# Optimization experiments

Measured on AMD Instinct MI355X. Metric: run time of the kernel, lower is better.

Reference implementation:

```python
import jax, jax.numpy as jnp
import numpy as np

D_MODEL = 1024
H = 16
D_K = D_MODEL // H
B, S = 2, 2048

def setup_inputs() -> dict:
    key = jax.random.key(0)
    ks = jax.random.split(key, 13)
    scale = 1.0 / np.sqrt(D_MODEL)
    mk = lambda k: jax.random.normal(k, (D_MODEL, D_MODEL), dtype=jnp.float32) * scale
    return {
        'q': jax.random.normal(ks[0], (B, S, D_MODEL), dtype=jnp.float32),
        'k': jax.random.normal(ks[1], (B, S, D_MODEL), dtype=jnp.float32),
        'v': jax.random.normal(ks[2], (B, S, D_MODEL), dtype=jnp.float32),
        'mask': jax.random.randint(ks[3], (B, 1, S, S), 0, 2, dtype=jnp.int32),
        'wq': mk(ks[4]), 'bq': jnp.zeros((D_MODEL,), jnp.float32),
        'wk': mk(ks[5]), 'bk': jnp.zeros((D_MODEL,), jnp.float32),
        'wv': mk(ks[6]), 'bv': jnp.zeros((D_MODEL,), jnp.float32),
        'wo': mk(ks[7]), 'bo': jnp.zeros((D_MODEL,), jnp.float32),
    }

def reference(q, k, v, mask, wq, bq, wk, bk, wv, bv, wo, bo):
    b, s, _ = q.shape
    # linear projections then split heads: [B,S,D] -> [B,H,S,Dk]
    def proj(x, w, bias):
        y = x @ w + bias
        return y.reshape(b, -1, H, D_K).transpose(0, 2, 1, 3)
    Q = proj(q, wq, bq)
    K = proj(k, wk, bk)
    V = proj(v, wv, bv)
    scores = jnp.einsum('bhqd,bhkd->bhqk', Q, K) / jnp.sqrt(jnp.float32(D_K))
    # faithful to source: masked positions are set to 1e-9 (not -inf)
    scores = jnp.where(mask == 0, jnp.float32(1e-9), scores)
    attn = jax.nn.softmax(scores, axis=-1)  # dropout is identity in eval mode
    x = jnp.einsum('bhqk,bhkd->bhqd', attn, V)
    x = x.transpose(0, 2, 1, 3).reshape(b, s, D_MODEL)
    return x @ wo + bo
```

## Files before the change

### kernel.cpp

```cpp
#include <hip/hip_runtime.h>
#include <hip/hip_bf16.h>

#define DM 1024
#define HEADS 16
#define DKK 64
#define BB 2
#define SS 2048
#define MROWS (BB*SS)

typedef __attribute__((ext_vector_type(8))) short bf16x8;
typedef __attribute__((ext_vector_type(4))) float f32x4;
typedef __hip_bfloat16 bf16;

#define SC2 0.1803368801f
#define MB2 1.442695041e-9f

__device__ __forceinline__ void async16(const void* g, void* l) {
    __builtin_amdgcn_global_load_lds((const __attribute__((address_space(1))) void*)g,
                                     (__attribute__((address_space(3))) void*)l, 16, 0, 0);
}

__global__ void prep_kernel(const float* __restrict__ q, const float* __restrict__ k,
                            const float* __restrict__ v,
                            const float* __restrict__ wq, const float* __restrict__ wk,
                            const float* __restrict__ wv, const float* __restrict__ wo,
                            const int* __restrict__ mask,
                            bf16* __restrict__ qkv, bf16* __restrict__ wcat,
                            unsigned long long* __restrict__ bits) {
    __shared__ float tile[32][33];
    const int bid = blockIdx.x;
    const int tid = threadIdx.x;
    if (bid < 12288) {
        const int z = bid >> 12;
        const int i = ((bid & 4095) << 8) + tid;
        const float* src = z == 0 ? q : (z == 1 ? k : v);
        float4 val = ((const float4*)src)[i];
        union { bf16 b[4]; ushort4 u; } cvt;
        cvt.b[0] = __float2bfloat16(val.x);
        cvt.b[1] = __float2bfloat16(val.y);
        cvt.b[2] = __float2bfloat16(val.z);
        cvt.b[3] = __float2bfloat16(val.w);
        ((ushort4*)(qkv + (size_t)z * MROWS * DM))[i] = cvt.u;
    } else if (bid < 12288 + 4096) {
        const int t = bid - 12288;
        const int z = t >> 10;
        const int bx = t & 31, by = (t >> 5) & 31;
        const float* src = z == 0 ? wq : (z == 1 ? wk : (z == 2 ? wv : wo));
        bf16* dst = wcat + ((size_t)z << 20);
        const int tx = tid & 31, ty = tid >> 5;
        const int x = bx * 32 + tx, y0 = by * 32 + ty;
#pragma unroll
        for (int i = 0; i < 32; i += 8)
            tile[ty + i][tx] = src[(size_t)(y0 + i) * DM + x];
        __syncthreads();
        const int nx = by * 32 + tx, ny0 = bx * 32 + ty;
#pragma unroll
        for (int i = 0; i < 32; i += 8)
            dst[(size_t)(ny0 + i) * DM + nx] = __float2bfloat16(tile[tx][ty + i]);
    } else {
        const int i = ((bid - 16384) << 8) + tid;
        unsigned long long b = __ballot(mask[i] != 0);
        if ((tid & 63) == 0) bits[i >> 6] = b;
    }
}

__global__ __launch_bounds__(256) void gemm_qkv(const bf16* __restrict__ qb, const bf16* __restrict__ kb,
                                                const bf16* __restrict__ vb, const bf16* __restrict__ wcat,
                                                const float* __restrict__ bq, const float* __restrict__ bk,
                                                const float* __restrict__ bv,
                                                bf16* __restrict__ Qh, bf16* __restrict__ Kh,
                                                bf16* __restrict__ Vt) {
    __shared__ __align__(16) bf16 lA[128 * 32];
    __shared__ __align__(16) bf16 lB[128 * 32];
    const int seg = blockIdx.x >> 3;
    const bf16* A    = seg == 0 ? qb : (seg == 1 ? kb : vb);
    const bf16* Bt   = wcat + ((size_t)seg << 20);
    const float* bias = seg == 0 ? bq : (seg == 1 ? bk : bv);

    const int tid  = threadIdx.x;
    const int lane = tid & 63;
    const int lm   = lane & 15;
    const int quad = lane >> 4;
    const int w    = tid >> 6;
    const int wm   = w >> 1, wn = w & 1;
    const int m0   = blockIdx.y * 128;
    const int n0   = (blockIdx.x & 7) * 128;
    const int wbase = w << 6;

    f32x4 acc[4][4];
#pragma unroll
    for (int i = 0; i < 4; ++i)
#pragma unroll
        for (int j = 0; j < 4; ++j) acc[i][j] = (f32x4){0.f, 0.f, 0.f, 0.f};

    for (int kt = 0; kt < DM / 32; ++kt) {
#pragma unroll
        for (int r = 0; r < 2; ++r) {
            const int idx = r * 256 + tid;
            const int row = idx >> 2;
            const int kc  = idx & 3;
            async16(A + (size_t)(m0 + row) * DM + kt * 32 + kc * 8,
                    (char*)lA + (size_t)(r * 256 + wbase) * 16);
            async16(Bt + (size_t)(n0 + row) * DM + kt * 32 + kc * 8,
                    (char*)lB + (size_t)(r * 256 + wbase) * 16);
        }
        __syncthreads();
        bf16x8 af[4], bb[4];
#pragma unroll
        for (int mt = 0; mt < 4; ++mt)
            af[mt] = *(const bf16x8*)&lA[(wm * 64 + mt * 16 + lm) * 32 + quad * 8];
#pragma unroll
        for (int nt = 0; nt < 4; ++nt)
            bb[nt] = *(const bf16x8*)&lB[(wn * 64 + nt * 16 + lm) * 32 + quad * 8];
#pragma unroll
        for (int mt = 0; mt < 4; ++mt)
#pragma unroll
            for (int nt = 0; nt < 4; ++nt)
                acc[mt][nt] = __builtin_amdgcn_mfma_f32_16x16x32_bf16(af[mt], bb[nt], acc[mt][nt], 0, 0, 0);
        __syncthreads();
    }

    bf16* outQK = seg == 0 ? Qh : Kh;
    const float oscale = (seg == 1) ? SC2 : 1.0f;
#pragma unroll
    for (int mt = 0; mt < 4; ++mt) {
#pragma unroll
        for (int nt = 0; nt < 4; ++nt) {
            const int gcol = n0 + wn * 64 + nt * 16 + lm;
            const float bvv = bias[gcol];
            const int h = gcol >> 6, d = gcol & 63;
#pragma unroll
            for (int r = 0; r < 4; ++r) {
                const int grow = m0 + wm * 64 + mt * 16 + quad * 4 + r;
                const int b = grow >> 11, s = grow & 2047;
                const float val = (acc[mt][nt][r] + bvv) * oscale;
                if (seg < 2)
                    outQK[((size_t)(b * HEADS + h) * SS + s) * DKK + d] = __float2bfloat16(val);
                else
                    Vt[((size_t)(b * HEADS + h) * DKK + d) * SS + s] = __float2bfloat16(val);
            }
        }
    }
}

__global__ __launch_bounds__(256) void gemm_out(const bf16* __restrict__ A, const bf16* __restrict__ Bt,
                                                const float* __restrict__ bias, float* __restrict__ outp) {
    __shared__ __align__(16) bf16 lA[128 * 32];
    __shared__ __align__(16) bf16 lB[64 * 32];
    const int tid  = threadIdx.x;
    const int lane = tid & 63;
    const int lm   = lane & 15;
    const int quad = lane >> 4;
    const int w    = tid >> 6;
    const int m0   = blockIdx.y * 128;
    const int n0   = blockIdx.x * 64;
    const int wbase = w << 6;

    f32x4 acc[2][4];
#pragma unroll
    for (int i = 0; i < 2; ++i)
#pragma unroll
        for (int j = 0; j < 4; ++j) acc[i][j] = (f32x4){0.f, 0.f, 0.f, 0.f};

    for (int kt = 0; kt < DM / 32; ++kt) {
#pragma unroll
        for (int r = 0; r < 2; ++r) {
            const int idx = r * 256 + tid;
            const int row = idx >> 2;
            const int kc  = idx & 3;
            async16(A + (size_t)(m0 + row) * DM + kt * 32 + kc * 8,
                    (char*)lA + (size_t)(r * 256 + wbase) * 16);
        }
        {
            const int row = tid >> 2;
            const int kc  = tid & 3;
            async16(Bt + (size_t)(n0 + row) * DM + kt * 32 + kc * 8,
                    (char*)lB + (size_t)(wbase) * 16);
        }
        __syncthreads();
        bf16x8 af[2], bb[4];
#pragma unroll
        for (int mt = 0; mt < 2; ++mt)
            af[mt] = *(const bf16x8*)&lA[(w * 32 + mt * 16 + lm) * 32 + quad * 8];
#pragma unroll
        for (int nt = 0; nt < 4; ++nt)
            bb[nt] = *(const bf16x8*)&lB[(nt * 16 + lm) * 32 + quad * 8];
#pragma unroll
        for (int mt = 0; mt < 2; ++mt)
#pragma unroll
            for (int nt = 0; nt < 4; ++nt)
                acc[mt][nt] = __builtin_amdgcn_mfma_f32_16x16x32_bf16(af[mt], bb[nt], acc[mt][nt], 0, 0, 0);
        __syncthreads();
    }

#pragma unroll
    for (int mt = 0; mt < 2; ++mt)
#pragma unroll
        for (int nt = 0; nt < 4; ++nt) {
            const int gcol = n0 + nt * 16 + lm;
            const float bvv = bias[gcol];
#pragma unroll
            for (int r = 0; r < 4; ++r) {
                const int grow = m0 + w * 32 + mt * 16 + quad * 4 + r;
                outp[(size_t)grow * DM + gcol] = acc[mt][nt][r] + bvv;
            }
        }
}

__global__ __launch_bounds__(256, 4) void attn_kernel(const bf16* __restrict__ Qh, const bf16* __restrict__ Kh,
                                                      const bf16* __restrict__ Vt,
                                                      const unsigned long long* __restrict__ mbits,
                                                      bf16* __restrict__ ctx) {
    __shared__ __align__(16) bf16 ldsK[2][64 * 64];
    __shared__ __align__(16) bf16 ldsV[2][64 * 64];
    __shared__ __align__(16) bf16 ldsP[4][16 * 64];

    const int tid  = threadIdx.x;
    const int lane = tid & 63;
    const int lm   = lane & 15;
    const int quad = lane >> 4;
    const int w    = tid >> 6;
    const int bh   = blockIdx.y;
    const int b    = bh >> 4;
    const int h    = bh & 15;
    const int q0   = blockIdx.x * 64;
    const int qrow = q0 + w * 16 + lm;

    const int x0 = quad ^ (lm & 7);
    const int x1 = x0 ^ 4;

    const int L0 = tid, L1 = 256 + tid;
    const int row0 = L0 >> 3, sw0 = (L0 & 7) ^ (row0 & 7);
    const int row1 = L1 >> 3, sw1 = (L1 & 7) ^ (row1 & 7);
    const bf16* kbase = Kh + (size_t)bh * SS * DKK;
    const bf16* vbase = Vt + (size_t)bh * DKK * SS;
    const bf16* pK0 = kbase + (size_t)row0 * DKK + sw0 * 8;
    const bf16* pK1 = kbase + (size_t)row1 * DKK + sw1 * 8;
    const bf16* pV0 = vbase + (size_t)row0 * SS + sw0 * 8;
    const bf16* pV1 = vbase + (size_t)row1 * SS + sw1 * 8;
    char* dKa[2] = { (char*)ldsK[0] + (size_t)(w * 64) * 16, (char*)ldsK[1] + (size_t)(w * 64) * 16 };
    char* dKb[2] = { (char*)ldsK[0] + (size_t)(256 + w * 64) * 16, (char*)ldsK[1] + (size_t)(256 + w * 64) * 16 };
    char* dVa[2] = { (char*)ldsV[0] + (size_t)(w * 64) * 16, (char*)ldsV[1] + (size_t)(w * 64) * 16 };
    char* dVb[2] = { (char*)ldsV[0] + (size_t)(256 + w * 64) * 16, (char*)ldsV[1] + (size_t)(256 + w * 64) * 16 };

    const bf16* qp = Qh + ((size_t)bh * SS + qrow) * DKK;
    const bf16x8 aq0 = *(const bf16x8*)(qp + quad * 8);
    const bf16x8 aq1 = *(const bf16x8*)(qp + 32 + quad * 8);

    const unsigned long long* pm = mbits + ((size_t)b * SS + qrow) * (SS / 64);

    f32x4 o[4];
#pragma unroll
    for (int i = 0; i < 4; ++i) o[i] = (f32x4){0.f, 0.f, 0.f, 0.f};
    float lsum = 0.f;
    bf16* pmy = &ldsP[w][0];

    async16(pK0, dKa[0]);
    async16(pK1, dKb[0]);
    async16(pV0, dVa[0]);
    async16(pV1, dVb[0]);
    __syncthreads();

    const int nkt = SS / 64;

    auto body = [&](int it, int cur) {
        const unsigned long long mw = pm[it];
        if (it + 1 < nkt) {
            const int nb = cur ^ 1;
            const size_t ko = (size_t)(it + 1) * 64;
            async16(pK0 + ko * DKK, dKa[nb]);
            async16(pK1 + ko * DKK, dKb[nb]);
            async16(pV0 + ko, dVa[nb]);
            async16(pV1 + ko, dVb[nb]);
        }
        const bf16* lk = ldsK[cur];
        const bf16* lv = ldsV[cur];

        f32x4 sc[4];
#pragma unroll
        for (int mt = 0; mt < 4; ++mt) {
            sc[mt] = (f32x4){0.f, 0.f, 0.f, 0.f};
            const bf16x8 kf0 = *(const bf16x8*)&lk[(mt * 16 + lm) * 64 + x0 * 8];
            const bf16x8 kf1 = *(const bf16x8*)&lk[(mt * 16 + lm) * 64 + x1 * 8];
            sc[mt] = __builtin_amdgcn_mfma_f32_16x16x32_bf16(kf0, aq0, sc[mt], 0, 0, 0);
            sc[mt] = __builtin_amdgcn_mfma_f32_16x16x32_bf16(kf1, aq1, sc[mt], 0, 0, 0);
        }

        const unsigned long long mq = mw >> (quad * 4);
#pragma unroll
        for (int mt = 0; mt < 4; ++mt) {
            const unsigned int mmt = (unsigned int)(mq >> (mt * 16));
            union { bf16 hh[4]; uint2 u; } pk;
#pragma unroll
            for (int r = 0; r < 4; ++r) {
                const float sv = ((mmt >> r) & 1u) ? sc[mt][r] : MB2;
                const float p = __builtin_amdgcn_exp2f(sv);
                lsum += p;
                pk.hh[r] = __float2bfloat16(p);
            }
            *(uint2*)&pmy[lm * 64 + (((mt * 2 + (quad >> 1)) ^ (lm & 7)) << 3) + ((quad & 1) << 2)] = pk.u;
        }

        const bf16x8 pf0 = *(const bf16x8*)&pmy[lm * 64 + x0 * 8];
        const bf16x8 pf1 = *(const bf16x8*)&pmy[lm * 64 + x1 * 8];
#pragma unroll
        for (int mt = 0; mt < 4; ++mt) {
            const bf16x8 vf0 = *(const bf16x8*)&lv[(mt * 16 + lm) * 64 + x0 * 8];
            const bf16x8 vf1 = *(const bf16x8*)&lv[(mt * 16 + lm) * 64 + x1 * 8];
            o[mt] = __builtin_amdgcn_mfma_f32_16x16x32_bf16(vf0, pf0, o[mt], 0, 0, 0);
            o[mt] = __builtin_amdgcn_mfma_f32_16x16x32_bf16(vf1, pf1, o[mt], 0, 0, 0);
        }

        __syncthreads();
    };

    for (int it = 0; it < nkt; it += 2) {
        body(it, 0);
        body(it + 1, 1);
    }

    lsum += __shfl_xor(lsum, 16);
    lsum += __shfl_xor(lsum, 32);
    const float rl = 1.0f / lsum;

    bf16* crow = ctx + ((size_t)b * SS + qrow) * DM + h * DKK;
#pragma unroll
    for (int mt = 0; mt < 4; ++mt) {
        union { bf16 hh[4]; uint2 u; } pk;
#pragma unroll
        for (int r = 0; r < 4; ++r) pk.hh[r] = __float2bfloat16(o[mt][r] * rl);
        *(uint2*)&crow[mt * 16 + quad * 4] = pk.u;
    }
}

extern "C" void kernel_launch(void* const* d_in, const int* in_sizes, int n_in,
                              void* d_out, int out_size, void* d_ws, size_t ws_size,
                              hipStream_t stream) {
    const float* q  = (const float*)d_in[0];
    const float* k  = (const float*)d_in[1];
    const float* v  = (const float*)d_in[2];
    const int* mask = (const int*)d_in[3];
    const float* wq = (const float*)d_in[4];
    const float* bq = (const float*)d_in[5];
    const float* wk = (const float*)d_in[6];
    const float* bk = (const float*)d_in[7];
    const float* wv = (const float*)d_in[8];
    const float* bv = (const float*)d_in[9];
    const float* wo = (const float*)d_in[10];
    const float* bo = (const float*)d_in[11];

    const size_t MB = 1ull << 20;
    char* ws = (char*)d_ws;
    bf16* qkv  = (bf16*)(ws + 0 * MB);
    bf16* wcat = (bf16*)(ws + 24 * MB);
    bf16* wot  = (bf16*)(ws + 30 * MB);
    bf16* Qh   = (bf16*)(ws + 32 * MB);
    bf16* Kh   = (bf16*)(ws + 40 * MB);
    bf16* Vt   = (bf16*)(ws + 48 * MB);
    bf16* ctx  = (bf16*)(ws + 56 * MB);
    unsigned long long* mbits = (unsigned long long*)(ws + 64 * MB);

    prep_kernel<<<49152, 256, 0, stream>>>(q, k, v, wq, wk, wv, wo, mask, qkv, wcat, mbits);

    gemm_qkv<<<dim3(24, 32), 256, 0, stream>>>(qkv, qkv + (size_t)MROWS * DM, qkv + 2 * (size_t)MROWS * DM,
                                               wcat, bq, bk, bv, Qh, Kh, Vt);

    attn_kernel<<<dim3(SS / 64, BB * HEADS), 256, 0, stream>>>(Qh, Kh, Vt, mbits, ctx);

    gemm_out<<<dim3(DM / 64, MROWS / 128), 256, 0, stream>>>(ctx, wot, bo, (float*)d_out);
}
```

Measured before the change: 273.4 us.

## Double-buffer GEMM LDS tiles and compute softmax row sums with MFMA

Both projection GEMMs now prefetch the next K tile into a second LDS buffer while computing on the current one, removing the per-iteration sync between issuing and consuming loads. In attention, the softmax denominator is accumulated via an extra MFMA with a ones operand instead of per-lane scalar adds and cross-lane shuffles. This costs double the LDS per GEMM block and two extra MFMAs per key tile.

```diff
diff --git a/kernel.cpp b/kernel.cpp
--- a/kernel.cpp
+++ b/kernel.cpp
@@ -70,8 +70,8 @@
                                                 const float* __restrict__ bv,
                                                 bf16* __restrict__ Qh, bf16* __restrict__ Kh,
                                                 bf16* __restrict__ Vt) {
-    __shared__ __align__(16) bf16 lA[128 * 32];
-    __shared__ __align__(16) bf16 lB[128 * 32];
+    __shared__ __align__(16) bf16 lA[2][128 * 32];
+    __shared__ __align__(16) bf16 lB[2][128 * 32];
     const int seg = blockIdx.x >> 3;
     const bf16* A    = seg == 0 ? qb : (seg == 1 ? kb : vb);
     const bf16* Bt   = wcat + ((size_t)seg << 20);
@@ -93,25 +93,33 @@
 #pragma unroll
         for (int j = 0; j < 4; ++j) acc[i][j] = (f32x4){0.f, 0.f, 0.f, 0.f};
 
-    for (int kt = 0; kt < DM / 32; ++kt) {
+    auto stage = [&](int kt, int buf) {
 #pragma unroll
         for (int r = 0; r < 2; ++r) {
             const int idx = r * 256 + tid;
             const int row = idx >> 2;
             const int kc  = idx & 3;
             async16(A + (size_t)(m0 + row) * DM + kt * 32 + kc * 8,
-                    (char*)lA + (size_t)(r * 256 + wbase) * 16);
+                    (char*)lA[buf] + (size_t)(r * 256 + wbase) * 16);
             async16(Bt + (size_t)(n0 + row) * DM + kt * 32 + kc * 8,
-                    (char*)lB + (size_t)(r * 256 + wbase) * 16);
-        }
-        __syncthreads();
+                    (char*)lB[buf] + (size_t)(r * 256 + wbase) * 16);
+        }
+    };
+
+    stage(0, 0);
+    __syncthreads();
+
+    const int nkt = DM / 32;
+    for (int kt = 0; kt < nkt; ++kt) {
+        const int cur = kt & 1;
+        if (kt + 1 < nkt) stage(kt + 1, cur ^ 1);
         bf16x8 af[4], bb[4];
 #pragma unroll
         for (int mt = 0; mt < 4; ++mt)
-            af[mt] = *(const bf16x8*)&lA[(wm * 64 + mt * 16 + lm) * 32 + quad * 8];
+            af[mt] = *(const bf16x8*)&lA[cur][(wm * 64 + mt * 16 + lm) * 32 + quad * 8];
 #pragma unroll
         for (int nt = 0; nt < 4; ++nt)
-            bb[nt] = *(const bf16x8*)&lB[(wn * 64 + nt * 16 + lm) * 32 + quad * 8];
+            bb[nt] = *(const bf16x8*)&lB[cur][(wn * 64 + nt * 16 + lm) * 32 + quad * 8];
 #pragma unroll
         for (int mt = 0; mt < 4; ++mt)
 #pragma unroll
@@ -145,8 +153,8 @@
 
 __global__ __launch_bounds__(256) void gemm_out(const bf16* __restrict__ A, const bf16* __restrict__ Bt,
                                                 const float* __restrict__ bias, float* __restrict__ outp) {
-    __shared__ __align__(16) bf16 lA[128 * 32];
-    __shared__ __align__(16) bf16 lB[64 * 32];
+    __shared__ __align__(16) bf16 lA[2][128 * 32];
+    __shared__ __align__(16) bf16 lB[2][64 * 32];
     const int tid  = threadIdx.x;
     const int lane = tid & 63;
     const int lm   = lane & 15;
@@ -162,29 +170,37 @@
 #pragma unroll
         for (int j = 0; j < 4; ++j) acc[i][j] = (f32x4){0.f, 0.f, 0.f, 0.f};
 
-    for (int kt = 0; kt < DM / 32; ++kt) {
+    auto stage = [&](int kt, int buf) {
 #pragma unroll
         for (int r = 0; r < 2; ++r) {
             const int idx = r * 256 + tid;
             const int row = idx >> 2;
             const int kc  = idx & 3;
             async16(A + (size_t)(m0 + row) * DM + kt * 32 + kc * 8,
-                    (char*)lA + (size_t)(r * 256 + wbase) * 16);
+                    (char*)lA[buf] + (size_t)(r * 256 + wbase) * 16);
         }
         {
             const int row = tid >> 2;
             const int kc  = tid & 3;
             async16(Bt + (size_t)(n0 + row) * DM + kt * 32 + kc * 8,
-                    (char*)lB + (size_t)(wbase) * 16);
-        }
-        __syncthreads();
+                    (char*)lB[buf] + (size_t)wbase * 16);
+        }
+    };
+
+    stage(0, 0);
+    __syncthreads();
+
+    const int nkt = DM / 32;
+    for (int kt = 0; kt < nkt; ++kt) {
+        const int cur = kt & 1;
+        if (kt + 1 < nkt) stage(kt + 1, cur ^ 1);
         bf16x8 af[2], bb[4];
 #pragma unroll
         for (int mt = 0; mt < 2; ++mt)
-            af[mt] = *(const bf16x8*)&lA[(w * 32 + mt * 16 + lm) * 32 + quad * 8];
+            af[mt] = *(const bf16x8*)&lA[cur][(w * 32 + mt * 16 + lm) * 32 + quad * 8];
 #pragma unroll
         for (int nt = 0; nt < 4; ++nt)
-            bb[nt] = *(const bf16x8*)&lB[(nt * 16 + lm) * 32 + quad * 8];
+            bb[nt] = *(const bf16x8*)&lB[cur][(nt * 16 + lm) * 32 + quad * 8];
 #pragma unroll
         for (int mt = 0; mt < 2; ++mt)
 #pragma unroll
@@ -249,10 +265,14 @@
 
     const unsigned long long* pm = mbits + ((size_t)b * SS + qrow) * (SS / 64);
 
+    const short one_bf16 = (short)0x3F80;
+    const bf16x8 onesf = (bf16x8){one_bf16, one_bf16, one_bf16, one_bf16,
+                                  one_bf16, one_bf16, one_bf16, one_bf16};
+
     f32x4 o[4];
 #pragma unroll
     for (int i = 0; i < 4; ++i) o[i] = (f32x4){0.f, 0.f, 0.f, 0.f};
-    float lsum = 0.f;
+    f32x4 o5 = (f32x4){0.f, 0.f, 0.f, 0.f};
     bf16* pmy = &ldsP[w][0];
 
     async16(pK0, dKa[0]);
@@ -294,9 +314,7 @@
 #pragma unroll
             for (int r = 0; r < 4; ++r) {
                 const float sv = ((mmt >> r) & 1u) ? sc[mt][r] : MB2;
-                const float p = __builtin_amdgcn_exp2f(sv);
-                lsum += p;
-                pk.hh[r] = __float2bfloat16(p);
+                pk.hh[r] = __float2bfloat16(__builtin_amdgcn_exp2f(sv));
             }
             *(uint2*)&pmy[lm * 64 + (((mt * 2 + (quad >> 1)) ^ (lm & 7)) << 3) + ((quad & 1) << 2)] = pk.u;
         }
@@ -310,6 +328,8 @@
             o[mt] = __builtin_amdgcn_mfma_f32_16x16x32_bf16(vf0, pf0, o[mt], 0, 0, 0);
             o[mt] = __builtin_amdgcn_mfma_f32_16x16x32_bf16(vf1, pf1, o[mt], 0, 0, 0);
         }
+        o5 = __builtin_amdgcn_mfma_f32_16x16x32_bf16(onesf, pf0, o5, 0, 0, 0);
+        o5 = __builtin_amdgcn_mfma_f32_16x16x32_bf16(onesf, pf1, o5, 0, 0, 0);
 
         __syncthreads();
     };
@@ -319,9 +339,7 @@
         body(it + 1, 1);
     }
 
-    lsum += __shfl_xor(lsum, 16);
-    lsum += __shfl_xor(lsum, 32);
-    const float rl = 1.0f / lsum;
+    const float rl = 1.0f / o5[0];
 
     bf16* crow = ctx + ((size_t)b * SS + qrow) * DM + h * DKK;
 #pragma unroll
```

After: 280.8 us. +2.7%, slower.

## Double attention query tile to 128 rows and compute row sums via MFMA

Applied to the files above, without the earlier changes.

The attention kernel now runs 512 threads (8 waves) per block, each block covering 128 query rows. Each K/V tile loaded into LDS is therefore shared by twice as many queries, and each thread issues one async load per tile instead of two. The softmax denominator is no longer accumulated with scalar adds and a cross-lane shuffle reduction. It comes from an extra MFMA against a ones vector using the bf16 probabilities, which adds two MFMAs per tile and sums bf16-rounded values instead of fp32 ones. The grid shrinks to half as many blocks, and the larger blocks may reduce occupancy.

```diff
diff --git a/kernel.cpp b/kernel.cpp
--- a/kernel.cpp
+++ b/kernel.cpp
@@ -175,7 +175,7 @@
             const int row = tid >> 2;
             const int kc  = tid & 3;
             async16(Bt + (size_t)(n0 + row) * DM + kt * 32 + kc * 8,
-                    (char*)lB + (size_t)(wbase) * 16);
+                    (char*)lB + (size_t)wbase * 16);
         }
         __syncthreads();
         bf16x8 af[2], bb[4];
@@ -207,13 +207,13 @@
         }
 }
 
-__global__ __launch_bounds__(256, 4) void attn_kernel(const bf16* __restrict__ Qh, const bf16* __restrict__ Kh,
+__global__ __launch_bounds__(512, 4) void attn_kernel(const bf16* __restrict__ Qh, const bf16* __restrict__ Kh,
                                                       const bf16* __restrict__ Vt,
                                                       const unsigned long long* __restrict__ mbits,
                                                       bf16* __restrict__ ctx) {
     __shared__ __align__(16) bf16 ldsK[2][64 * 64];
     __shared__ __align__(16) bf16 ldsV[2][64 * 64];
-    __shared__ __align__(16) bf16 ldsP[4][16 * 64];
+    __shared__ __align__(16) bf16 ldsP[8][16 * 64];
 
     const int tid  = threadIdx.x;
     const int lane = tid & 63;
@@ -223,25 +223,19 @@
     const int bh   = blockIdx.y;
     const int b    = bh >> 4;
     const int h    = bh & 15;
-    const int q0   = blockIdx.x * 64;
+    const int q0   = blockIdx.x * 128;
     const int qrow = q0 + w * 16 + lm;
 
     const int x0 = quad ^ (lm & 7);
     const int x1 = x0 ^ 4;
 
-    const int L0 = tid, L1 = 256 + tid;
-    const int row0 = L0 >> 3, sw0 = (L0 & 7) ^ (row0 & 7);
-    const int row1 = L1 >> 3, sw1 = (L1 & 7) ^ (row1 & 7);
+    const int row = tid >> 3, sw = (tid & 7) ^ (row & 7);
     const bf16* kbase = Kh + (size_t)bh * SS * DKK;
     const bf16* vbase = Vt + (size_t)bh * DKK * SS;
-    const bf16* pK0 = kbase + (size_t)row0 * DKK + sw0 * 8;
-    const bf16* pK1 = kbase + (size_t)row1 * DKK + sw1 * 8;
-    const bf16* pV0 = vbase + (size_t)row0 * SS + sw0 * 8;
-    const bf16* pV1 = vbase + (size_t)row1 * SS + sw1 * 8;
-    char* dKa[2] = { (char*)ldsK[0] + (size_t)(w * 64) * 16, (char*)ldsK[1] + (size_t)(w * 64) * 16 };
-    char* dKb[2] = { (char*)ldsK[0] + (size_t)(256 + w * 64) * 16, (char*)ldsK[1] + (size_t)(256 + w * 64) * 16 };
-    char* dVa[2] = { (char*)ldsV[0] + (size_t)(w * 64) * 16, (char*)ldsV[1] + (size_t)(w * 64) * 16 };
-    char* dVb[2] = { (char*)ldsV[0] + (size_t)(256 + w * 64) * 16, (char*)ldsV[1] + (size_t)(256 + w * 64) * 16 };
+    const bf16* pK = kbase + (size_t)row * DKK + sw * 8;
+    const bf16* pV = vbase + (size_t)row * SS + sw * 8;
+    char* dK[2] = { (char*)ldsK[0] + (size_t)w * 1024, (char*)ldsK[1] + (size_t)w * 1024 };
+    char* dV[2] = { (char*)ldsV[0] + (size_t)w * 1024, (char*)ldsV[1] + (size_t)w * 1024 };
 
     const bf16* qp = Qh + ((size_t)bh * SS + qrow) * DKK;
     const bf16x8 aq0 = *(const bf16x8*)(qp + quad * 8);
@@ -249,16 +243,18 @@
 
     const unsigned long long* pm = mbits + ((size_t)b * SS + qrow) * (SS / 64);
 
+    const short one_bf16 = (short)0x3F80;
+    const bf16x8 onesf = (bf16x8){one_bf16, one_bf16, one_bf16, one_bf16,
+                                  one_bf16, one_bf16, one_bf16, one_bf16};
+
     f32x4 o[4];
 #pragma unroll
     for (int i = 0; i < 4; ++i) o[i] = (f32x4){0.f, 0.f, 0.f, 0.f};
-    float lsum = 0.f;
+    f32x4 o5 = (f32x4){0.f, 0.f, 0.f, 0.f};
     bf16* pmy = &ldsP[w][0];
 
-    async16(pK0, dKa[0]);
-    async16(pK1, dKb[0]);
-    async16(pV0, dVa[0]);
-    async16(pV1, dVb[0]);
+    async16(pK, dK[0]);
+    async16(pV, dV[0]);
     __syncthreads();
 
     const int nkt = SS / 64;
@@ -268,10 +264,8 @@
         if (it + 1 < nkt) {
             const int nb = cur ^ 1;
             const size_t ko = (size_t)(it + 1) * 64;
-            async16(pK0 + ko * DKK, dKa[nb]);
-            async16(pK1 + ko * DKK, dKb[nb]);
-            async16(pV0 + ko, dVa[nb]);
-            async16(pV1 + ko, dVb[nb]);
+            async16(pK + ko * DKK, dK[nb]);
+            async16(pV + ko, dV[nb]);
         }
         const bf16* lk = ldsK[cur];
         const bf16* lv = ldsV[cur];
@@ -294,9 +288,7 @@
 #pragma unroll
             for (int r = 0; r < 4; ++r) {
                 const float sv = ((mmt >> r) & 1u) ? sc[mt][r] : MB2;
-                const float p = __builtin_amdgcn_exp2f(sv);
-                lsum += p;
-                pk.hh[r] = __float2bfloat16(p);
+                pk.hh[r] = __float2bfloat16(__builtin_amdgcn_exp2f(sv));
             }
             *(uint2*)&pmy[lm * 64 + (((mt * 2 + (quad >> 1)) ^ (lm & 7)) << 3) + ((quad & 1) << 2)] = pk.u;
         }
@@ -310,6 +302,8 @@
             o[mt] = __builtin_amdgcn_mfma_f32_16x16x32_bf16(vf0, pf0, o[mt], 0, 0, 0);
             o[mt] = __builtin_amdgcn_mfma_f32_16x16x32_bf16(vf1, pf1, o[mt], 0, 0, 0);
         }
+        o5 = __builtin_amdgcn_mfma_f32_16x16x32_bf16(onesf, pf0, o5, 0, 0, 0);
+        o5 = __builtin_amdgcn_mfma_f32_16x16x32_bf16(onesf, pf1, o5, 0, 0, 0);
 
         __syncthreads();
     };
@@ -319,9 +313,7 @@
         body(it + 1, 1);
     }
 
-    lsum += __shfl_xor(lsum, 16);
-    lsum += __shfl_xor(lsum, 32);
-    const float rl = 1.0f / lsum;
+    const float rl = 1.0f / o5[0];
 
     bf16* crow = ctx + ((size_t)b * SS + qrow) * DM + h * DKK;
 #pragma unroll
@@ -365,7 +357,7 @@
     gemm_qkv<<<dim3(24, 32), 256, 0, stream>>>(qkv, qkv + (size_t)MROWS * DM, qkv + 2 * (size_t)MROWS * DM,
                                                wcat, bq, bk, bv, Qh, Kh, Vt);
 
-    attn_kernel<<<dim3(SS / 64, BB * HEADS), 256, 0, stream>>>(Qh, Kh, Vt, mbits, ctx);
+    attn_kernel<<<dim3(SS / 128, BB * HEADS), 512, 0, stream>>>(Qh, Kh, Vt, mbits, ctx);
 
     gemm_out<<<dim3(DM / 64, MROWS / 128), 256, 0, stream>>>(ctx, wot, bo, (float*)d_out);
 }
```

Measured after the change: 275.2 us. About the same (+0.7%).

## Process 32 query rows per wave in attention and compute row sums via MFMA

Applied to the files above, without the earlier changes.

The attention kernel now gives each wave 32 query rows instead of 16, so a block covers 128 queries. Each K/V tile loaded into LDS is reused across twice as many queries, and the grid is halved. The softmax denominator is now computed with an extra MFMA against a ones vector over the bf16 P tile, replacing the scalar accumulation and cross-lane shuffles. The cost is more registers (launch bounds lowered to 2), a larger P buffer in LDS, fewer blocks for occupancy, and a denominator computed from bf16-rounded probabilities.

```diff
diff --git a/kernel.cpp b/kernel.cpp
--- a/kernel.cpp
+++ b/kernel.cpp
@@ -175,7 +175,7 @@
             const int row = tid >> 2;
             const int kc  = tid & 3;
             async16(Bt + (size_t)(n0 + row) * DM + kt * 32 + kc * 8,
-                    (char*)lB + (size_t)(wbase) * 16);
+                    (char*)lB + (size_t)wbase * 16);
         }
         __syncthreads();
         bf16x8 af[2], bb[4];
@@ -207,13 +207,13 @@
         }
 }
 
-__global__ __launch_bounds__(256, 4) void attn_kernel(const bf16* __restrict__ Qh, const bf16* __restrict__ Kh,
+__global__ __launch_bounds__(256, 2) void attn_kernel(const bf16* __restrict__ Qh, const bf16* __restrict__ Kh,
                                                       const bf16* __restrict__ Vt,
                                                       const unsigned long long* __restrict__ mbits,
                                                       bf16* __restrict__ ctx) {
     __shared__ __align__(16) bf16 ldsK[2][64 * 64];
     __shared__ __align__(16) bf16 ldsV[2][64 * 64];
-    __shared__ __align__(16) bf16 ldsP[4][16 * 64];
+    __shared__ __align__(16) bf16 ldsP[4][32 * 64];
 
     const int tid  = threadIdx.x;
     const int lane = tid & 63;
@@ -223,8 +223,7 @@
     const int bh   = blockIdx.y;
     const int b    = bh >> 4;
     const int h    = bh & 15;
-    const int q0   = blockIdx.x * 64;
-    const int qrow = q0 + w * 16 + lm;
+    const int q0   = blockIdx.x * 128;
 
     const int x0 = quad ^ (lm & 7);
     const int x1 = x0 ^ 4;
@@ -243,16 +242,27 @@
     char* dVa[2] = { (char*)ldsV[0] + (size_t)(w * 64) * 16, (char*)ldsV[1] + (size_t)(w * 64) * 16 };
     char* dVb[2] = { (char*)ldsV[0] + (size_t)(256 + w * 64) * 16, (char*)ldsV[1] + (size_t)(256 + w * 64) * 16 };
 
-    const bf16* qp = Qh + ((size_t)bh * SS + qrow) * DKK;
-    const bf16x8 aq0 = *(const bf16x8*)(qp + quad * 8);
-    const bf16x8 aq1 = *(const bf16x8*)(qp + 32 + quad * 8);
-
-    const unsigned long long* pm = mbits + ((size_t)b * SS + qrow) * (SS / 64);
-
-    f32x4 o[4];
-#pragma unroll
-    for (int i = 0; i < 4; ++i) o[i] = (f32x4){0.f, 0.f, 0.f, 0.f};
-    float lsum = 0.f;
+    bf16x8 aq[2][2];
+#pragma unroll
+    for (int nt = 0; nt < 2; ++nt) {
+        const bf16* qp = Qh + ((size_t)bh * SS + q0 + w * 32 + nt * 16 + lm) * DKK;
+        aq[nt][0] = *(const bf16x8*)(qp + quad * 8);
+        aq[nt][1] = *(const bf16x8*)(qp + 32 + quad * 8);
+    }
+
+    const unsigned long long* pm0 = mbits + ((size_t)b * SS + q0 + w * 32 + lm) * (SS / 64);
+    const unsigned long long* pm1 = pm0 + 16 * (SS / 64);
+
+    const short one_bf16 = (short)0x3F80;
+    const bf16x8 onesf = (bf16x8){one_bf16, one_bf16, one_bf16, one_bf16,
+                                  one_bf16, one_bf16, one_bf16, one_bf16};
+
+    f32x4 o[4][2];
+#pragma unroll
+    for (int i = 0; i < 4; ++i)
+#pragma unroll
+        for (int j = 0; j < 2; ++j) o[i][j] = (f32x4){0.f, 0.f, 0.f, 0.f};
+    f32x4 o5[2] = {(f32x4){0.f, 0.f, 0.f, 0.f}, (f32x4){0.f, 0.f, 0.f, 0.f}};
     bf16* pmy = &ldsP[w][0];
 
     async16(pK0, dKa[0]);
@@ -264,7 +274,8 @@
     const int nkt = SS / 64;
 
     auto body = [&](int it, int cur) {
-        const unsigned long long mw = pm[it];
+        const unsigned long long mw0 = pm0[it];
+        const unsigned long long mw1 = pm1[it];
         if (it + 1 < nkt) {
             const int nb = cur ^ 1;
             const size_t ko = (size_t)(it + 1) * 64;
@@ -276,39 +287,56 @@
         const bf16* lk = ldsK[cur];
         const bf16* lv = ldsV[cur];
 
-        f32x4 sc[4];
+        f32x4 sc[4][2];
 #pragma unroll
         for (int mt = 0; mt < 4; ++mt) {
-            sc[mt] = (f32x4){0.f, 0.f, 0.f, 0.f};
             const bf16x8 kf0 = *(const bf16x8*)&lk[(mt * 16 + lm) * 64 + x0 * 8];
             const bf16x8 kf1 = *(const bf16x8*)&lk[(mt * 16 + lm) * 64 + x1 * 8];
-            sc[mt] = __builtin_amdgcn_mfma_f32_16x16x32_bf16(kf0, aq0, sc[mt], 0, 0, 0);
-            sc[mt] = __builtin_amdgcn_mfma_f32_16x16x32_bf16(kf1, aq1, sc[mt], 0, 0, 0);
-        }
-
-        const unsigned long long mq = mw >> (quad * 4);
+#pragma unroll
+            for (int nt = 0; nt < 2; ++nt) {
+                sc[mt][nt] = (f32x4){0.f, 0.f, 0.f, 0.f};
+                sc[mt][nt] = __builtin_amdgcn_mfma_f32_16x16x32_bf16(kf0, aq[nt][0], sc[mt][nt], 0, 0, 0);
+                sc[mt][nt] = __builtin_amdgcn_mfma_f32_16x16x32_bf16(kf1, aq[nt][1], sc[mt][nt], 0, 0, 0);
+            }
+        }
+
+        const unsigned long long mq0 = mw0 >> (quad * 4);
+        const unsigned long long mq1 = mw1 >> (quad * 4);
 #pragma unroll
         for (int mt = 0; mt < 4; ++mt) {
-            const unsigned int mmt = (unsigned int)(mq >> (mt * 16));
-            union { bf16 hh[4]; uint2 u; } pk;
-#pragma unroll
-            for (int r = 0; r < 4; ++r) {
-                const float sv = ((mmt >> r) & 1u) ? sc[mt][r] : MB2;
-                const float p = __builtin_amdgcn_exp2f(sv);
-                lsum += p;
-                pk.hh[r] = __float2bfloat16(p);
+#pragma unroll
+            for (int nt = 0; nt < 2; ++nt) {
+                const unsigned int mmt = (unsigned int)((nt ? mq1 : mq0) >> (mt * 16));
+                union { bf16 hh[4]; uint2 u; } pk;
+#pragma unroll
+                for (int r = 0; r < 4; ++r) {
+                    const float sv = ((mmt >> r) & 1u) ? sc[mt][nt][r] : MB2;
+                    pk.hh[r] = __float2bfloat16(__builtin_amdgcn_exp2f(sv));
+                }
+                *(uint2*)&pmy[(nt * 16 + lm) * 64 + (((mt * 2 + (quad >> 1)) ^ (lm & 7)) << 3) + ((quad & 1) << 2)] = pk.u;
             }
-            *(uint2*)&pmy[lm * 64 + (((mt * 2 + (quad >> 1)) ^ (lm & 7)) << 3) + ((quad & 1) << 2)] = pk.u;
-        }
-
-        const bf16x8 pf0 = *(const bf16x8*)&pmy[lm * 64 + x0 * 8];
-        const bf16x8 pf1 = *(const bf16x8*)&pmy[lm * 64 + x1 * 8];
+        }
+
+        bf16x8 pf[2][2];
+#pragma unroll
+        for (int kc = 0; kc < 2; ++kc)
+#pragma unroll
+            for (int nt = 0; nt < 2; ++nt)
+                pf[kc][nt] = *(const bf16x8*)&pmy[(nt * 16 + lm) * 64 + (((kc * 4 + quad) ^ (lm & 7)) << 3)];
 #pragma unroll
         for (int mt = 0; mt < 4; ++mt) {
             const bf16x8 vf0 = *(const bf16x8*)&lv[(mt * 16 + lm) * 64 + x0 * 8];
             const bf16x8 vf1 = *(const bf16x8*)&lv[(mt * 16 + lm) * 64 + x1 * 8];
-            o[mt] = __builtin_amdgcn_mfma_f32_16x16x32_bf16(vf0, pf0, o[mt], 0, 0, 0);
-            o[mt] = __builtin_amdgcn_mfma_f32_16x16x32_bf16(vf1, pf1, o[mt], 0, 0, 0);
+#pragma unroll
+            for (int nt = 0; nt < 2; ++nt) {
+                o[mt][nt] = __builtin_amdgcn_mfma_f32_16x16x32_bf16(vf0, pf[0][nt], o[mt][nt], 0, 0, 0);
+                o[mt][nt] = __builtin_amdgcn_mfma_f32_16x16x32_bf16(vf1, pf[1][nt], o[mt][nt], 0, 0, 0);
+            }
+        }
+#pragma unroll
+        for (int nt = 0; nt < 2; ++nt) {
+            o5[nt] = __builtin_amdgcn_mfma_f32_16x16x32_bf16(onesf, pf[0][nt], o5[nt], 0, 0, 0);
+            o5[nt] = __builtin_amdgcn_mfma_f32_16x16x32_bf16(onesf, pf[1][nt], o5[nt], 0, 0, 0);
         }
 
         __syncthreads();
@@ -319,17 +347,18 @@
         body(it + 1, 1);
     }
 
-    lsum += __shfl_xor(lsum, 16);
-    lsum += __shfl_xor(lsum, 32);
-    const float rl = 1.0f / lsum;
-
-    bf16* crow = ctx + ((size_t)b * SS + qrow) * DM + h * DKK;
-#pragma unroll
-    for (int mt = 0; mt < 4; ++mt) {
-        union { bf16 hh[4]; uint2 u; } pk;
-#pragma unroll
-        for (int r = 0; r < 4; ++r) pk.hh[r] = __float2bfloat16(o[mt][r] * rl);
-        *(uint2*)&crow[mt * 16 + quad * 4] = pk.u;
+    const float rl[2] = { 1.0f / o5[0][0], 1.0f / o5[1][0] };
+
+#pragma unroll
+    for (int nt = 0; nt < 2; ++nt) {
+        bf16* crow = ctx + ((size_t)b * SS + q0 + w * 32 + nt * 16 + lm) * DM + h * DKK;
+#pragma unroll
+        for (int mt = 0; mt < 4; ++mt) {
+            union { bf16 hh[4]; uint2 u; } pk;
+#pragma unroll
+            for (int r = 0; r < 4; ++r) pk.hh[r] = __float2bfloat16(o[mt][nt][r] * rl[nt]);
+            *(uint2*)&crow[mt * 16 + quad * 4] = pk.u;
+        }
     }
 }
 
@@ -365,7 +394,7 @@
     gemm_qkv<<<dim3(24, 32), 256, 0, stream>>>(qkv, qkv + (size_t)MROWS * DM, qkv + 2 * (size_t)MROWS * DM,
                                                wcat, bq, bk, bv, Qh, Kh, Vt);
 
-    attn_kernel<<<dim3(SS / 64, BB * HEADS), 256, 0, stream>>>(Qh, Kh, Vt, mbits, ctx);
+    attn_kernel<<<dim3(SS / 128, BB * HEADS), 256, 0, stream>>>(Qh, Kh, Vt, mbits, ctx);
 
     gemm_out<<<dim3(DM / 64, MROWS / 128), 256, 0, stream>>>(ctx, wot, bo, (float*)d_out);
 }
```

Measured after the change: 275.8 us. About the same (+0.9%).
